# Optimization experiments

Measured on AMD Instinct MI355X. Metric: run time of the kernel, lower is better.

Reference implementation:

```python
import jax, jax.numpy as jnp
import numpy as np

H = 1024
S = 2048
B = 16

def setup_inputs() -> dict:
    key = jax.random.key(0)
    k1, k2, k3, k4, k5, k6 = jax.random.split(key, 6)
    hidden = jax.random.normal(k1, (1, B, H), dtype=jnp.float32)
    encoder_outputs = jax.random.normal(k2, (S, B, H), dtype=jnp.float32)
    seq_mask = jax.random.randint(k3, (B, S), 0, 2, dtype=jnp.int32)
    # nn.Linear(2H, H): weight [H, 2H], bias [H]
    lim1 = 1.0 / np.sqrt(2 * H)
    attn_w = jax.random.uniform(k4, (H, 2 * H), minval=-lim1, maxval=lim1, dtype=jnp.float32)
    attn_b = jax.random.uniform(k5, (H,), minval=-lim1, maxval=lim1, dtype=jnp.float32)
    # nn.Linear(H, 1, bias=False): weight [1, H]
    lim2 = 1.0 / np.sqrt(H)
    score_w = jax.random.uniform(k6, (1, H), minval=-lim2, maxval=lim2, dtype=jnp.float32)
    return {"hidden": hidden, "encoder_outputs": encoder_outputs, "seq_mask": seq_mask,
            "attn_w": attn_w, "attn_b": attn_b, "score_w": score_w}

def reference(hidden, encoder_outputs, seq_mask, attn_w, attn_b, score_w):
    # Faithful to: cat([hidden.repeat(S,1,1), encoder_outputs], -1) @ attn_w.T + attn_b
    # Split the concat-linear into two GEMMs (identical math, avoids the big concat).
    h = hidden.shape[-1]
    Wh = attn_w[:, :h]   # acts on repeated hidden
    We = attn_w[:, h:]   # acts on encoder outputs
    # hidden: [1,B,H] broadcasts over S; encoder_outputs: [S,B,H]
    pre = jnp.einsum('obh,kh->obk', hidden, Wh) + jnp.einsum('sbh,kh->sbk', encoder_outputs, We) + attn_b
    proj = jnp.tanh(pre)                               # [S,B,H]
    energies = jnp.einsum('sbh,oh->sbo', proj, score_w)[..., 0]  # [S,B]
    energies = energies.T                              # [B,S] (transpose(0,1) in original)
    energies = jnp.where(seq_mask.astype(bool), jnp.float32(-1e12), energies)
    attn = jax.nn.softmax(energies, axis=1)            # [B,S]
    return attn[:, None, :]                            # [B,1,S]
```

## Files before the change

kernel.cpp:

```cpp
#include <hip/hip_runtime.h>
#include <hip/hip_bf16.h>

#define HDIM 1024
#define SEQ 2048
#define BATCH 16
#define M_TOT (SEQ*BATCH)
#define NBLK 4
#define BM 256
#define BN 256
#define BKT 64
#define NT (HDIM/BKT)

#define NB_ENC ((M_TOT*HDIM)/(8*256))
#define NB_WE  ((HDIM*HDIM)/(8*256))
#define NB_QK  (HDIM)

typedef __attribute__((ext_vector_type(8))) short short8;
typedef __attribute__((ext_vector_type(4))) float f32x4;

typedef const void __attribute__((address_space(1))) gvoid_t;
typedef void __attribute__((address_space(3))) svoid_t;
#define GLD16(gp, lp) __builtin_amdgcn_global_load_lds((gvoid_t*)(gp), (svoid_t*)(lp), 16, 0, 0)
#define VMC(N) asm volatile("s_waitcnt vmcnt(" #N ")" ::: "memory")

static __device__ __forceinline__ unsigned short f2bf(float f) {
    unsigned int x = __float_as_uint(f);
    unsigned int r = (x + 0x7FFFu + ((x >> 16) & 1u)) >> 16;
    return (unsigned short)r;
}

__global__ __launch_bounds__(1024) void scan_kernel(const int* __restrict__ mask,
                                                    int* __restrict__ rowidx,
                                                    int* __restrict__ jof,
                                                    int* __restrict__ nkeep) {
    int t = threadIdx.x;
    int base = t * 32;
    unsigned flags = 0;
    int cnt = 0;
    const int4* m4 = reinterpret_cast<const int4*>(mask + base);
#pragma unroll
    for (int v = 0; v < 8; ++v) {
        int4 x = m4[v];
        if (x.x == 0) { flags |= 1u << (v * 4 + 0); cnt++; }
        if (x.y == 0) { flags |= 1u << (v * 4 + 1); cnt++; }
        if (x.z == 0) { flags |= 1u << (v * 4 + 2); cnt++; }
        if (x.w == 0) { flags |= 1u << (v * 4 + 3); cnt++; }
    }
    int lane = t & 63, wv = t >> 6;
    int inc = cnt;
    for (int off = 1; off < 64; off <<= 1) {
        int o = __shfl_up(inc, off);
        if (lane >= off) inc += o;
    }
    __shared__ int wsum[16], wbase[16];
    if (lane == 63) wsum[wv] = inc;
    __syncthreads();
    if (t == 0) {
        int acc = 0;
        for (int w = 0; w < 16; ++w) { wbase[w] = acc; acc += wsum[w]; }
        nkeep[0] = acc;
    }
    __syncthreads();
    int e = wbase[wv] + inc - cnt;
#pragma unroll
    for (int i = 0; i < 32; ++i) {
        if ((flags >> i) & 1u) {
            int l = base + i;
            int m = ((l & 2047) << 4) | (l >> 11);
            rowidx[e] = m;
            jof[m] = e;
            e++;
        }
    }
}

__global__ __launch_bounds__(256) void prep_all(const float* __restrict__ hidden,
                                                const float* __restrict__ enc,
                                                const float* __restrict__ attn_w,
                                                const float* __restrict__ attn_b,
                                                const int* __restrict__ rowidx,
                                                const int* __restrict__ nkp,
                                                float* __restrict__ q,
                                                __hip_bfloat16* __restrict__ web,
                                                __hip_bfloat16* __restrict__ encb) {
    int bid = blockIdx.x;
    if (bid < NB_ENC) {
        int nkeep = nkp[0];
        int npad = (nkeep + 255) & ~255;
        int j = bid * 2 + (threadIdx.x >> 7);
        if (j >= npad) return;
        int col = (threadIdx.x & 127) * 8;
        unsigned short* dst = (unsigned short*)encb + (size_t)j * HDIM + col;
        if (j >= nkeep) {
            short8 z = (short8)0;
            *reinterpret_cast<short8*>(dst) = z;
            return;
        }
        int m = rowidx[j];
        const float4* s4 = reinterpret_cast<const float4*>(enc + (size_t)m * HDIM + col);
        float4 a = s4[0], b = s4[1];
        union { unsigned short u[8]; short8 v; } cv;
        cv.u[0] = f2bf(a.x); cv.u[1] = f2bf(a.y); cv.u[2] = f2bf(a.z); cv.u[3] = f2bf(a.w);
        cv.u[4] = f2bf(b.x); cv.u[5] = f2bf(b.y); cv.u[6] = f2bf(b.z); cv.u[7] = f2bf(b.w);
        *reinterpret_cast<short8*>(dst) = cv.v;
        return;
    }
    if (bid < NB_ENC + NB_WE) {
        size_t i0 = ((size_t)(bid - NB_ENC) * 256 + threadIdx.x) * 8;
        int n = (int)(i0 >> 10);
        int h = (int)(i0 & 1023);
        const float4* src = reinterpret_cast<const float4*>(attn_w + (size_t)n * (2 * HDIM) + HDIM + h);
        float4 a = src[0], b = src[1];
        union { unsigned short u[8]; short8 v; } cv;
        cv.u[0] = f2bf(a.x); cv.u[1] = f2bf(a.y); cv.u[2] = f2bf(a.z); cv.u[3] = f2bf(a.w);
        cv.u[4] = f2bf(b.x); cv.u[5] = f2bf(b.y); cv.u[6] = f2bf(b.z); cv.u[7] = f2bf(b.w);
        *reinterpret_cast<short8*>((unsigned short*)web + i0) = cv.v;
        return;
    }
    int k = bid - (NB_ENC + NB_WE);
    int tid = threadIdx.x;
    const float* w = attn_w + (size_t)k * (2 * HDIM);
    float p[BATCH];
#pragma unroll
    for (int b = 0; b < BATCH; b++) p[b] = 0.f;
    for (int h = tid; h < HDIM; h += 256) {
        float wv = w[h];
#pragma unroll
        for (int b = 0; b < BATCH; b++) p[b] += hidden[b * HDIM + h] * wv;
    }
#pragma unroll
    for (int b = 0; b < BATCH; b++) {
        for (int off = 32; off; off >>= 1) p[b] += __shfl_down(p[b], off);
    }
    __shared__ float red[4][BATCH];
    int lane = tid & 63, wid = tid >> 6;
    if (lane == 0) {
#pragma unroll
        for (int b = 0; b < BATCH; b++) red[wid][b] = p[b];
    }
    __syncthreads();
    if (tid < BATCH) {
        float s = red[0][tid] + red[1][tid] + red[2][tid] + red[3][tid] + attn_b[k];
        q[(size_t)tid * HDIM + k] = s;
    }
}

__global__ __launch_bounds__(512, 2) void gemm8(const __hip_bfloat16* __restrict__ encb,
                                                const __hip_bfloat16* __restrict__ web,
                                                const float* __restrict__ qv,
                                                const float* __restrict__ score_w,
                                                const int* __restrict__ rowidx,
                                                const int* __restrict__ nkp,
                                                float* __restrict__ part) {
    __shared__ __align__(16) char pool[163840];

    int tid = threadIdx.x;
    int lane = tid & 63;
    int wid = tid >> 6;
    int wr = wid >> 2;
    int wc = wid & 3;

    int bid = blockIdx.x;
    int bm = ((bid >> 5) << 3) | (bid & 7);
    int bn = (bid >> 3) & 3;
    int m0 = bm * BM, n0 = bn * BN;

    int nkeep = nkp[0];
    int npad = (nkeep + 255) & ~255;
    if (m0 >= npad) return;

    int srow = tid >> 3;
    int scolb = (((tid & 7) ^ ((tid >> 3) & 7)) << 4);
    const char* eb = (const char*)encb;
    const char* wb = (const char*)web;

    auto STG = [&](const char* g, int ldsoff) {
        GLD16(g + (size_t)srow * 2048 + scolb, pool + ldsoff + wid * 1024);
        GLD16(g + (size_t)(srow + 64) * 2048 + scolb, pool + ldsoff + 8192 + wid * 1024);
    };
    auto APTR = [&](int kt, int h) { return eb + ((size_t)(m0 + h * 128) * HDIM + kt * BKT) * 2; };
    auto BPTR = [&](int kt, int h) { return wb + ((size_t)(n0 + h * 128) * HDIM + kt * BKT) * 2; };
#define ALDS(par, h) ((par) * 32768 + (h) * 16384)
#define BLDS(buf, h) (65536 + (buf) * 32768 + (h) * 16384)

    int lq = lane & 15, lh = lane >> 4;
    int flip = (lane & 7) << 4;
    int pks0 = lq * 128 + ((lh * 16) ^ flip);
    int pks1 = lq * 128 + (((64 + lh * 16)) ^ flip);
    int aFB = wr * 16384;
    int bOFF = (wc >> 1) * 16384 + (wc & 1) * 8192;

    f32x4 acc[8][4];
#pragma unroll
    for (int i = 0; i < 8; i++)
#pragma unroll
        for (int j = 0; j < 4; j++) acc[i][j] = (f32x4)0.f;
    short8 br[4][2];

#define RD8(off) (*reinterpret_cast<const short8*>(pool + (off)))

#define CLUSTER(Q, PAR, BB, STAGE_STMT)                                                   \
    {                                                                                     \
        if ((Q) == 0) {                                                                   \
            _Pragma("unroll") for (int nj = 0; nj < 4; ++nj) {                            \
                br[nj][0] = RD8(65536 + (BB) * 32768 + bOFF + nj * 2048 + pks0);          \
                br[nj][1] = RD8(65536 + (BB) * 32768 + bOFF + nj * 2048 + pks1);          \
            }                                                                             \
        }                                                                                 \
        short8 a0k0 = RD8(aFB + (PAR) * 32768 + (2 * (Q)) * 2048 + pks0);                 \
        short8 a0k1 = RD8(aFB + (PAR) * 32768 + (2 * (Q)) * 2048 + pks1);                 \
        short8 a1k0 = RD8(aFB + (PAR) * 32768 + (2 * (Q) + 1) * 2048 + pks0);             \
        short8 a1k1 = RD8(aFB + (PAR) * 32768 + (2 * (Q) + 1) * 2048 + pks1);             \
        STAGE_STMT;                                                                       \
        __builtin_amdgcn_s_setprio(1);                                                    \
        _Pragma("unroll") for (int nj = 0; nj < 4; ++nj) {                                \
            acc[2 * (Q)][nj] = __builtin_amdgcn_mfma_f32_16x16x32_bf16(a0k0, br[nj][0], acc[2 * (Q)][nj], 0, 0, 0); \
            acc[2 * (Q)][nj] = __builtin_amdgcn_mfma_f32_16x16x32_bf16(a0k1, br[nj][1], acc[2 * (Q)][nj], 0, 0, 0); \
            acc[2 * (Q) + 1][nj] = __builtin_amdgcn_mfma_f32_16x16x32_bf16(a1k0, br[nj][0], acc[2 * (Q) + 1][nj], 0, 0, 0); \
            acc[2 * (Q) + 1][nj] = __builtin_amdgcn_mfma_f32_16x16x32_bf16(a1k1, br[nj][1], acc[2 * (Q) + 1][nj], 0, 0, 0); \
        }                                                                                 \
        __builtin_amdgcn_s_setprio(0);                                                    \
    }

#define TILE(PAR, BB, S1, S2, S3, S4, CLOSE)                                              \
    {                                                                                     \
        CLUSTER(0, PAR, BB, S1);                                                          \
        CLUSTER(1, PAR, BB, S2);                                                          \
        CLUSTER(2, PAR, BB, S3);                                                          \
        CLUSTER(3, PAR, BB, S4);                                                          \
        CLOSE;                                                                            \
        __builtin_amdgcn_s_barrier();                                                     \
        __builtin_amdgcn_sched_barrier(0);                                                \
    }

    STG(APTR(0, 0), ALDS(0, 0));
    STG(APTR(0, 1), ALDS(0, 1));
    STG(BPTR(0, 0), BLDS(0, 0));
    STG(BPTR(0, 1), BLDS(0, 1));
    STG(BPTR(1, 0), BLDS(1, 0));
    STG(BPTR(1, 1), BLDS(1, 1));
    VMC(4);
    __builtin_amdgcn_s_barrier();
    __builtin_amdgcn_sched_barrier(0);

#pragma unroll 1
    for (int J = 0; J < 2; ++J) {
        int t = 6 * J;
        TILE(0, 0, STG(APTR(t + 1, 0), ALDS(1, 0)), STG(APTR(t + 1, 1), ALDS(1, 1)),
                   STG(BPTR(t + 2, 0), BLDS(2, 0)), STG(BPTR(t + 2, 1), BLDS(2, 1)), VMC(4));
        TILE(1, 1, STG(APTR(t + 2, 0), ALDS(0, 0)), STG(APTR(t + 2, 1), ALDS(0, 1)),
                   STG(BPTR(t + 3, 0), BLDS(0, 0)), STG(BPTR(t + 3, 1), BLDS(0, 1)), VMC(4));
        TILE(0, 2, STG(APTR(t + 3, 0), ALDS(1, 0)), STG(APTR(t + 3, 1), ALDS(1, 1)),
                   STG(BPTR(t + 4, 0), BLDS(1, 0)), STG(BPTR(t + 4, 1), BLDS(1, 1)), VMC(4));
        TILE(1, 0, STG(APTR(t + 4, 0), ALDS(0, 0)), STG(APTR(t + 4, 1), ALDS(0, 1)),
                   STG(BPTR(t + 5, 0), BLDS(2, 0)), STG(BPTR(t + 5, 1), BLDS(2, 1)), VMC(4));
        TILE(0, 1, STG(APTR(t + 5, 0), ALDS(1, 0)), STG(APTR(t + 5, 1), ALDS(1, 1)),
                   STG(BPTR(t + 6, 0), BLDS(0, 0)), STG(BPTR(t + 6, 1), BLDS(0, 1)), VMC(4));
        TILE(1, 2, STG(APTR(t + 6, 0), ALDS(0, 0)), STG(APTR(t + 6, 1), ALDS(0, 1)),
                   STG(BPTR(t + 7, 0), BLDS(1, 0)), STG(BPTR(t + 7, 1), BLDS(1, 1)), VMC(4));
    }
    TILE(0, 0, STG(APTR(13, 0), ALDS(1, 0)), STG(APTR(13, 1), ALDS(1, 1)),
               STG(BPTR(14, 0), BLDS(2, 0)), STG(BPTR(14, 1), BLDS(2, 1)), VMC(4));
    TILE(1, 1, STG(APTR(14, 0), ALDS(0, 0)), STG(APTR(14, 1), ALDS(0, 1)),
               STG(BPTR(15, 0), BLDS(0, 0)), STG(BPTR(15, 1), BLDS(0, 1)), VMC(4));
    TILE(0, 2, STG(APTR(15, 0), ALDS(1, 0)), STG(APTR(15, 1), ALDS(1, 1)), , , VMC(0));
    TILE(1, 0, , , , , );

    float* q_lds = reinterpret_cast<float*>(pool);
    float* sc_lds = reinterpret_cast<float*>(pool + 16384);
    int* rowb = reinterpret_cast<int*>(pool + 17408);
    float* red = reinterpret_cast<float*>(pool + 18432);
    {
        int qb = tid >> 5;
        int kl = (tid & 31) * 8;
        const float4* src = reinterpret_cast<const float4*>(qv + (size_t)qb * HDIM + n0 + kl);
        float4 v0 = src[0], v1 = src[1];
        *reinterpret_cast<float4*>(&q_lds[qb * 256 + kl]) = v0;
        *reinterpret_cast<float4*>(&q_lds[qb * 256 + kl + 4]) = v1;
        if (tid < BN) sc_lds[tid] = score_w[n0 + tid];
        if (tid < BM) rowb[tid] = (m0 + tid < nkeep) ? (rowidx[m0 + tid] & 15) : 0;
    }
    __syncthreads();

#pragma unroll
    for (int mi = 0; mi < 8; ++mi) {
#pragma unroll
        for (int r = 0; r < 4; ++r) {
            int row = wr * 128 + mi * 16 + lh * 4 + r;
            int bq = rowb[row];
            float s = 0.f;
#pragma unroll
            for (int nj = 0; nj < 4; ++nj) {
                int kl = wc * 64 + nj * 16 + lq;
                float v = acc[mi][nj][r] + q_lds[bq * 256 + kl];
                float t = 1.f - 2.f / (__expf(2.f * v) + 1.f);
                s += sc_lds[kl] * t;
            }
            red[(wc * 256 + row) * 20 + lq] = s;
        }
    }
    __syncthreads();
    if (tid < BM) {
        float t = 0.f;
#pragma unroll
        for (int w4 = 0; w4 < 4; ++w4) {
            const f32x4* p = reinterpret_cast<const f32x4*>(&red[(w4 * 256 + tid) * 20]);
#pragma unroll
            for (int i = 0; i < 4; ++i) {
                f32x4 v = p[i];
                t += v[0] + v[1] + v[2] + v[3];
            }
        }
        part[(size_t)bn * M_TOT + m0 + tid] = t;
    }
#undef CLUSTER
#undef TILE
#undef RD8
#undef ALDS
#undef BLDS
}

__global__ __launch_bounds__(256) void softmax_kernel(const float* __restrict__ part,
                                                      const int* __restrict__ mask,
                                                      const int* __restrict__ jof,
                                                      float* __restrict__ out) {
    int b = blockIdx.x;
    int tid = threadIdx.x;
    __shared__ float e_lds[SEQ];
    __shared__ float red[4], red2[4];
    int lane = tid & 63, wid = tid >> 6;
    float lmax = -3.4e38f;
    for (int it = 0; it < SEQ / 256; ++it) {
        int s = it * 256 + tid;
        float e = -1e12f;
        if (!mask[(size_t)b * SEQ + s]) {
            int m = s * BATCH + b;
            int j = jof[m];
            float acc = 0.f;
#pragma unroll
            for (int c = 0; c < NBLK; c++) acc += part[(size_t)c * M_TOT + j];
            e = acc;
        }
        e_lds[s] = e;
        lmax = fmaxf(lmax, e);
    }
    for (int off = 32; off; off >>= 1) lmax = fmaxf(lmax, __shfl_xor(lmax, off));
    if (lane == 0) red[wid] = lmax;
    __syncthreads();
    float gmax = fmaxf(fmaxf(red[0], red[1]), fmaxf(red[2], red[3]));
    float lsum = 0.f;
    for (int it = 0; it < SEQ / 256; ++it) {
        int s = it * 256 + tid;
        float p = __expf(e_lds[s] - gmax);
        e_lds[s] = p;
        lsum += p;
    }
    for (int off = 32; off; off >>= 1) lsum += __shfl_xor(lsum, off);
    if (lane == 0) red2[wid] = lsum;
    __syncthreads();
    float inv = 1.f / (red2[0] + red2[1] + red2[2] + red2[3]);
    for (int it = 0; it < SEQ / 256; ++it) {
        int s = it * 256 + tid;
        out[(size_t)b * SEQ + s] = e_lds[s] * inv;
    }
}

extern "C" void kernel_launch(void* const* d_in, const int* in_sizes, int n_in,
                              void* d_out, int out_size, void* d_ws, size_t ws_size,
                              hipStream_t stream) {
    const float* hidden   = (const float*)d_in[0];
    const float* enc      = (const float*)d_in[1];
    const int*   seq_mask = (const int*)d_in[2];
    const float* attn_w   = (const float*)d_in[3];
    const float* attn_b   = (const float*)d_in[4];
    const float* score_w  = (const float*)d_in[5];
    float* out = (float*)d_out;

    char* ws = (char*)d_ws;
    float* q = (float*)ws;
    __hip_bfloat16* web = (__hip_bfloat16*)(ws + 65536);
    float* part = (float*)(ws + 65536 + 2 * 1024 * 1024);
    int* rowidx = (int*)(ws + 65536 + 2 * 1024 * 1024 + 512 * 1024);
    int* jof    = (int*)(ws + 65536 + 2 * 1024 * 1024 + 640 * 1024);
    int* nkeep  = (int*)(ws + 65536 + 2 * 1024 * 1024 + 768 * 1024);
    __hip_bfloat16* encb = (__hip_bfloat16*)(ws + 65536 + 3 * 1024 * 1024);

    scan_kernel<<<dim3(1), dim3(1024), 0, stream>>>(seq_mask, rowidx, jof, nkeep);
    prep_all<<<dim3(NB_ENC + NB_WE + NB_QK), dim3(256), 0, stream>>>(hidden, enc, attn_w, attn_b,
                                                                     rowidx, nkeep, q, web, encb);
    gemm8<<<dim3(NBLK * (M_TOT / BM)), dim3(512), 0, stream>>>(encb, web, q, score_w,
                                                               rowidx, nkeep, part);
    softmax_kernel<<<dim3(BATCH), dim3(256), 0, stream>>>(part, seq_mask, jof, out);
}
```

Measured before the change: 123.7 us.

## Split GEMM into a fixed one-wave main grid plus a small remainder kernel

The main GEMM now always covers exactly the first 16384 compacted rows with 256 blocks, which is meant to be one full wave on the device. Any kept rows beyond that go to a new lightweight MFMA kernel that works on 32-row tiles. That kernel also applies tanh, the score dot product and the partial reduction, and writes the same partial-energy buffer. The goal is to remove the tail wave of a few extra large blocks, which happens because the unmasked row count lands slightly above a multiple of the grid capacity. The block-to-tile mapping is also reshuffled, and the prep kernel zero-pads rows up to 16384 so the fixed grid reads valid data. The cost is an extra kernel launch, and the remainder kernel loads operands straight from global memory with no LDS reuse.

```diff
diff --git a/kernel.cpp b/kernel.cpp
--- a/kernel.cpp
+++ b/kernel.cpp
@@ -10,6 +10,7 @@
 #define BN 256
 #define BKT 64
 #define NT (HDIM/BKT)
+#define MMAIN 16384
 
 #define NB_ENC ((M_TOT*HDIM)/(8*256))
 #define NB_WE  ((HDIM*HDIM)/(8*256))
@@ -87,8 +88,9 @@
     if (bid < NB_ENC) {
         int nkeep = nkp[0];
         int npad = (nkeep + 255) & ~255;
+        int plim = npad > MMAIN ? npad : MMAIN;
         int j = bid * 2 + (threadIdx.x >> 7);
-        if (j >= npad) return;
+        if (j >= plim) return;
         int col = (threadIdx.x & 127) * 8;
         unsigned short* dst = (unsigned short*)encb + (size_t)j * HDIM + col;
         if (j >= nkeep) {
@@ -161,13 +163,12 @@
     int wc = wid & 3;
 
     int bid = blockIdx.x;
-    int bm = ((bid >> 5) << 3) | (bid & 7);
-    int bn = (bid >> 3) & 3;
+    int lin = (bid & 7) * 32 + (bid >> 3);
+    int bm = lin >> 2;
+    int bn = lin & 3;
     int m0 = bm * BM, n0 = bn * BN;
 
     int nkeep = nkp[0];
-    int npad = (nkeep + 255) & ~255;
-    if (m0 >= npad) return;
 
     int srow = tid >> 3;
     int scolb = (((tid & 7) ^ ((tid >> 3) & 7)) << 4);
@@ -320,6 +321,68 @@
 #undef BLDS
 }
 
+__global__ __launch_bounds__(256) void rem_kernel(const __hip_bfloat16* __restrict__ encb,
+                                                  const __hip_bfloat16* __restrict__ web,
+                                                  const float* __restrict__ qv,
+                                                  const float* __restrict__ score_w,
+                                                  const int* __restrict__ rowidx,
+                                                  const int* __restrict__ nkp,
+                                                  float* __restrict__ part) {
+    int nkeep = nkp[0];
+    int bid = blockIdx.x;
+    int mt = bid >> 2, bn = bid & 3;
+    int j0 = MMAIN + mt * 32;
+    if (j0 >= nkeep) return;
+
+    int tid = threadIdx.x, lane = tid & 63, w = tid >> 6;
+    int lq = lane & 15, lh = lane >> 4;
+    int colblk = bn * 256 + w * 64;
+
+    f32x4 acc[2][4];
+#pragma unroll
+    for (int i = 0; i < 2; i++)
+#pragma unroll
+        for (int j = 0; j < 4; j++) acc[i][j] = (f32x4)0.f;
+
+    for (int kt = 0; kt < 32; ++kt) {
+        int kb = kt * 32 + lh * 8;
+        short8 a0 = *reinterpret_cast<const short8*>(encb + (size_t)(j0 + lq) * HDIM + kb);
+        short8 a1 = *reinterpret_cast<const short8*>(encb + (size_t)(j0 + 16 + lq) * HDIM + kb);
+#pragma unroll
+        for (int nj = 0; nj < 4; ++nj) {
+            short8 b = *reinterpret_cast<const short8*>(web + (size_t)(colblk + nj * 16 + lq) * HDIM + kb);
+            acc[0][nj] = __builtin_amdgcn_mfma_f32_16x16x32_bf16(a0, b, acc[0][nj], 0, 0, 0);
+            acc[1][nj] = __builtin_amdgcn_mfma_f32_16x16x32_bf16(a1, b, acc[1][nj], 0, 0, 0);
+        }
+    }
+
+    __shared__ float eng[4][32];
+#pragma unroll
+    for (int mi = 0; mi < 2; ++mi) {
+#pragma unroll
+        for (int r = 0; r < 4; ++r) {
+            int row = mi * 16 + lh * 4 + r;
+            int j = j0 + row;
+            int bq = (j < nkeep) ? (rowidx[j] & 15) : 0;
+            float s = 0.f;
+#pragma unroll
+            for (int nj = 0; nj < 4; ++nj) {
+                int kl = colblk + nj * 16 + lq;
+                float v = acc[mi][nj][r] + qv[(size_t)bq * HDIM + kl];
+                float t = 1.f - 2.f / (__expf(2.f * v) + 1.f);
+                s += score_w[kl] * t;
+            }
+            for (int off = 1; off < 16; off <<= 1) s += __shfl_xor(s, off);
+            if (lq == 0) eng[w][row] = s;
+        }
+    }
+    __syncthreads();
+    if (tid < 32) {
+        float t = eng[0][tid] + eng[1][tid] + eng[2][tid] + eng[3][tid];
+        part[(size_t)bn * M_TOT + j0 + tid] = t;
+    }
+}
+
 __global__ __launch_bounds__(256) void softmax_kernel(const float* __restrict__ part,
                                                       const int* __restrict__ mask,
                                                       const int* __restrict__ jof,
@@ -388,7 +451,7 @@
     scan_kernel<<<dim3(1), dim3(1024), 0, stream>>>(seq_mask, rowidx, jof, nkeep);
     prep_all<<<dim3(NB_ENC + NB_WE + NB_QK), dim3(256), 0, stream>>>(hidden, enc, attn_w, attn_b,
                                                                      rowidx, nkeep, q, web, encb);
-    gemm8<<<dim3(NBLK * (M_TOT / BM)), dim3(512), 0, stream>>>(encb, web, q, score_w,
-                                                               rowidx, nkeep, part);
+    gemm8<<<dim3(256), dim3(512), 0, stream>>>(encb, web, q, score_w, rowidx, nkeep, part);
+    rem_kernel<<<dim3(2048), dim3(256), 0, stream>>>(encb, web, q, score_w, rowidx, nkeep, part);
     softmax_kernel<<<dim3(BATCH), dim3(256), 0, stream>>>(part, seq_mask, jof, out);
 }
```

New measurement: 123.1 us. Within noise of the previous version (-0.5%).
